# Performance work log

Hardware: AMD Instinct MI355X
Metric: run time of the kernel (lower is better)

## Reference

```python
import jax, jax.numpy as jnp
import numpy as np

N_NODES = 10000
N_EDGES = 320000
IN_DIM = 256
OUT_DIM = 256
N_REL = 16


def setup_inputs() -> dict:
    key = jax.random.key(0)
    k_x, k_src, k_dst, k_et, k_wr, k_w0 = jax.random.split(key, 6)
    x = jax.random.normal(k_x, (N_NODES, IN_DIM), dtype=jnp.float32)
    src = jax.random.randint(k_src, (N_EDGES,), 0, N_NODES)
    dst = jax.random.randint(k_dst, (N_EDGES,), 0, N_NODES)
    edge_index = jnp.stack([src, dst], axis=0)  # [2, E]
    edge_type = jax.random.randint(k_et, (N_EDGES,), 0, N_REL)
    # Xavier-uniform-ish init for weights
    lim_r = float(np.sqrt(6.0 / (IN_DIM + OUT_DIM)))
    W_r = jax.random.uniform(k_wr, (N_REL, IN_DIM, OUT_DIM), minval=-lim_r, maxval=lim_r, dtype=jnp.float32)
    W0_w = jax.random.uniform(k_w0, (OUT_DIM, IN_DIM), minval=-lim_r, maxval=lim_r, dtype=jnp.float32)
    W0_b = jnp.zeros((OUT_DIM,), dtype=jnp.float32)
    return {
        "x": x,
        "W_r": W_r,
        "W0_w": W0_w,
        "W0_b": W0_b,
        "edge_index": edge_index,
        "edge_type": edge_type,
        "num_nodes_local": N_NODES,
    }


def reference(x, W_r, W0_w, W0_b, edge_index, edge_type, num_nodes_local):
    N = num_nodes_local
    R = W_r.shape[0]
    src = edge_index[0]
    dst = edge_index[1]
    # Per-(relation, dst-node) in-degree, clamped at 1 (matches deg_r.clamp_min(1))
    deg = jnp.zeros((R, N), dtype=x.dtype).at[edge_type, dst].add(1.0)
    deg = jnp.maximum(deg, 1.0)  # [R, N]
    # Transform all nodes under every relation weight: grouped GEMM [R, N, out]
    h_all = jnp.einsum('nd,rdo->rno', x, W_r)
    # Gather per-edge message and normalize by relation-specific dst degree
    msg = h_all[edge_type, src] / deg[edge_type, dst][:, None]  # [E, out]
    # Scatter-add messages to destination nodes
    agg = jax.ops.segment_sum(msg, dst, num_segments=N)  # [N, out]
    # Self-loop transform W_0(x)
    return agg + x @ W0_w.T + W0_b
```

## Files before the change

kernel.cpp:

```cpp
#include <hip/hip_runtime.h>

typedef __bf16 bf16x8 __attribute__((ext_vector_type(8)));
typedef float f32x4 __attribute__((ext_vector_type(4)));

static __device__ __forceinline__ unsigned short f2bf(float f) {
    union { float f; unsigned int u; } v; v.f = f;
    unsigned int r = v.u + 0x7fffu + ((v.u >> 16) & 1u);
    return (unsigned short)(r >> 16);
}
static __device__ __forceinline__ float blo(unsigned int u) {
    union { unsigned int u; float f; } v; v.u = u << 16; return v.f;
}
static __device__ __forceinline__ float bhi(unsigned int u) {
    union { unsigned int u; float f; } v; v.u = u & 0xffff0000u; return v.f;
}
static __device__ __forceinline__ unsigned int pack2(float a, float b) {
    return (unsigned int)f2bf(a) | ((unsigned int)f2bf(b) << 16);
}

__global__ void zero_kernel(int* __restrict__ p, int n) {
    int i = blockIdx.x * blockDim.x + threadIdx.x;
    int n4 = n >> 2;
    if (i < n4) reinterpret_cast<int4*>(p)[i] = make_int4(0, 0, 0, 0);
    if (i < (n & 3)) p[(n4 << 2) + i] = 0;
}

__global__ void prep_kernel(const int* __restrict__ dst, const int* __restrict__ et,
                            int* __restrict__ deg,
                            const float* __restrict__ x, unsigned short* __restrict__ s,
                            int E, int N, int R, int nh) {
    const int bid = blockIdx.x, tid = threadIdx.x;
    const int K = (R + 1) * 256;
    if (bid < nh) {
        int i = bid * 256 + tid;
        if (i < E) atomicAdd(&deg[et[i] * N + dst[i]], 1);
    } else {
        int id = (bid - nh) * 256 + tid;
        int n = id >> 6, c4 = id & 63;
        if (n < N) {
            float4 v = *reinterpret_cast<const float4*>(&x[((size_t)n << 8) + (c4 << 2)]);
            ushort4 h;
            h.x = f2bf(v.x); h.y = f2bf(v.y); h.z = f2bf(v.z); h.w = f2bf(v.w);
            *reinterpret_cast<ushort4*>(&s[(size_t)n * K + (K - 256) + (c4 << 2)]) = h;
        }
    }
}

__global__ __launch_bounds__(256) void wtT_kernel(
    const float* __restrict__ Wr, const float* __restrict__ W0w,
    unsigned short* __restrict__ Wt2, int R, int K)
{
    __shared__ float t[64][65];
    const int sl = blockIdx.x, d0 = blockIdx.y * 64, o0 = blockIdx.z * 64;
    const int tid = threadIdx.x;
    if (sl < R) {
        #pragma unroll
        for (int j = 0; j < 16; ++j) {
            int idx = j * 256 + tid;
            int dr = idx >> 6, oc = idx & 63;
            t[dr][oc] = Wr[((size_t)sl * 256 + d0 + dr) * 256 + o0 + oc];
        }
        __syncthreads();
        #pragma unroll
        for (int j = 0; j < 4; ++j) {
            int idx = j * 256 + tid;
            int orow = idx >> 4, dc4 = (idx & 15) << 2;
            ushort4 h;
            h.x = f2bf(t[dc4 + 0][orow]); h.y = f2bf(t[dc4 + 1][orow]);
            h.z = f2bf(t[dc4 + 2][orow]); h.w = f2bf(t[dc4 + 3][orow]);
            *reinterpret_cast<ushort4*>(&Wt2[(size_t)(o0 + orow) * K + sl * 256 + d0 + dc4]) = h;
        }
    } else {
        #pragma unroll
        for (int j = 0; j < 4; ++j) {
            int idx = j * 256 + tid;
            int orow = idx >> 4, dc4 = (idx & 15) << 2;
            float4 v = *reinterpret_cast<const float4*>(&W0w[(size_t)(o0 + orow) * 256 + d0 + dc4]);
            ushort4 h;
            h.x = f2bf(v.x); h.y = f2bf(v.y); h.z = f2bf(v.z); h.w = f2bf(v.w);
            *reinterpret_cast<ushort4*>(&Wt2[(size_t)(o0 + orow) * K + sl * 256 + d0 + dc4]) = h;
        }
    }
}

__global__ void scan1_kernel(const int* __restrict__ deg, int* __restrict__ local,
                             int* __restrict__ bsum, int* __restrict__ ctr, int B) {
    __shared__ int tmp[256];
    int t = threadIdx.x, g = blockIdx.x * 256 + t;
    int v = (g < B) ? deg[g] : 0;
    tmp[t] = v; __syncthreads();
    for (int o = 1; o < 256; o <<= 1) {
        int u = (t >= o) ? tmp[t - o] : 0;
        __syncthreads();
        tmp[t] += u;
        __syncthreads();
    }
    if (g < B) { local[g] = tmp[t] - v; ctr[g] = 0; }
    if (t == 255) bsum[blockIdx.x] = tmp[t];
}

__global__ void scan2_kernel(const int* __restrict__ bsum, int* __restrict__ base, int nc) {
    __shared__ int tmp[1024];
    int t = threadIdx.x;
    int v = (t < nc) ? bsum[t] : 0;
    tmp[t] = v; __syncthreads();
    for (int o = 1; o < 1024; o <<= 1) {
        int u = (t >= o) ? tmp[t - o] : 0;
        __syncthreads();
        tmp[t] += u;
        __syncthreads();
    }
    if (t < nc) base[t] = tmp[t] - v;
}

__global__ void scatter_ids_kernel(const int* __restrict__ src, const int* __restrict__ dst,
                                   const int* __restrict__ et, const int* __restrict__ local,
                                   const int* __restrict__ base, int* __restrict__ ctr,
                                   int* __restrict__ srcs, int E, int N) {
    int i = blockIdx.x * blockDim.x + threadIdx.x;
    if (i < E) {
        int b = et[i] * N + dst[i];
        int p = local[b] + base[b >> 8] + atomicAdd(&ctr[b], 1);
        srcs[p] = src[i];
    }
}

__global__ __launch_bounds__(256) void reduce_kernel(
    const int* __restrict__ srcs, const int* __restrict__ deg,
    const int* __restrict__ local, const int* __restrict__ base,
    unsigned short* __restrict__ s, int N, int R)
{
    const int K = (R + 1) * 256;
    const int r = blockIdx.y;
    const int dn = blockIdx.x * 8 + (threadIdx.x >> 5);
    if (dn >= N) return;
    const int lane = threadIdx.x & 31;
    const int bin = r * N + dn;
    const int cnt = deg[bin];
    const int st  = local[bin] + base[bin >> 8];

    float a0 = 0.f, a1 = 0.f, a2 = 0.f, a3 = 0.f;
    float a4 = 0.f, a5 = 0.f, a6 = 0.f, a7 = 0.f;
    for (int c0 = 0; c0 < cnt; c0 += 32) {
        int sv = 0;
        if (c0 + lane < cnt) sv = srcs[st + c0 + lane];
        int m = cnt - c0; if (m > 32) m = 32;
        for (int i = 0; i < m; ++i) {
            int sn = __shfl(sv, i, 32);
            const uint4 v = *reinterpret_cast<const uint4*>(
                &s[(size_t)sn * K + (K - 256) + (lane << 3)]);
            a0 += blo(v.x); a1 += bhi(v.x);
            a2 += blo(v.y); a3 += bhi(v.y);
            a4 += blo(v.z); a5 += bhi(v.z);
            a6 += blo(v.w); a7 += bhi(v.w);
        }
    }
    if (cnt > 0) {
        float sc = 1.0f / (float)cnt;
        a0 *= sc; a1 *= sc; a2 *= sc; a3 *= sc;
        a4 *= sc; a5 *= sc; a6 *= sc; a7 *= sc;
    }
    uint4 o;
    o.x = pack2(a0, a1); o.y = pack2(a2, a3);
    o.z = pack2(a4, a5); o.w = pack2(a6, a7);
    *reinterpret_cast<uint4*>(&s[(size_t)dn * K + (r << 8) + (lane << 3)]) = o;
}

__global__ __launch_bounds__(256) void gemm_kernel(
    const unsigned short* __restrict__ S, const unsigned short* __restrict__ Wt2,
    const float* __restrict__ bias, float* __restrict__ dest,
    int M, int K, int ksteps, int addbias)
{
    __shared__ __align__(16) unsigned short ldsA[2][8192];
    __shared__ __align__(16) unsigned short ldsB[8192];
    const int tid = threadIdx.x;
    const int lane = tid & 63, w = tid >> 6;
    const int wm = w & 1, wn = w >> 1;
    const int m0 = blockIdx.x * 128, n0 = blockIdx.y * 128;
    const int kstart = blockIdx.z * ksteps * 64;
    const size_t rowb = (size_t)K * 2;

    f32x4 acc[4][4] = {};

    const int flat_base = w * 4 * 64 + lane;

#define STAGE_A(buf, kstep)                                                               \
    {                                                                                     \
        const int kb = (kstart + (kstep) * 64) * 2;                                       \
        _Pragma("unroll")                                                                 \
        for (int i = 0; i < 4; ++i) {                                                     \
            int flat = flat_base + i * 64;                                                \
            int row = flat >> 3, seg = flat & 7;                                          \
            int gr = m0 + row; gr = gr < M ? gr : M - 1;                                  \
            const char* gp = (const char*)S + (size_t)gr * rowb + kb                      \
                             + ((seg * 16) ^ ((row & 7) << 4));                           \
            unsigned short* lp = &ldsA[buf][(w * 4 + i) * 512];                           \
            __builtin_amdgcn_global_load_lds(                                             \
                (const __attribute__((address_space(1))) void*)gp,                        \
                (__attribute__((address_space(3))) void*)lp, 16, 0, 0);                   \
        }                                                                                 \
    }

#define STAGE_B(kstep)                                                                    \
    {                                                                                     \
        const int kb = (kstart + (kstep) * 64) * 2;                                       \
        _Pragma("unroll")                                                                 \
        for (int i = 0; i < 4; ++i) {                                                     \
            int flat = flat_base + i * 64;                                                \
            int row = flat >> 3, seg = flat & 7;                                          \
            const char* gp = (const char*)Wt2 + (size_t)(n0 + row) * rowb + kb            \
                             + ((seg * 16) ^ ((row & 7) << 4));                           \
            unsigned short* lp = &ldsB[(w * 4 + i) * 512];                                \
            __builtin_amdgcn_global_load_lds(                                             \
                (const __attribute__((address_space(1))) void*)gp,                        \
                (__attribute__((address_space(3))) void*)lp, 16, 0, 0);                   \
        }                                                                                 \
    }

#define COMPUTE(buf)                                                                      \
    {                                                                                     \
        _Pragma("unroll")                                                                 \
        for (int kk = 0; kk < 2; ++kk) {                                                  \
            bf16x8 af[4], bfr[4];                                                         \
            _Pragma("unroll")                                                             \
            for (int m = 0; m < 4; ++m) {                                                 \
                int row = wm * 64 + m * 16 + (lane & 15);                                 \
                int colb = (kk * 64 + ((lane >> 4) << 4)) ^ ((row & 7) << 4);             \
                af[m] = *reinterpret_cast<const bf16x8*>(                                 \
                    (const char*)&ldsA[buf][0] + row * 128 + colb);                       \
            }                                                                             \
            _Pragma("unroll")                                                             \
            for (int n = 0; n < 4; ++n) {                                                 \
                int row = wn * 64 + n * 16 + (lane & 15);                                 \
                int colb = (kk * 64 + ((lane >> 4) << 4)) ^ ((row & 7) << 4);             \
                bfr[n] = *reinterpret_cast<const bf16x8*>(                                \
                    (const char*)&ldsB[0] + row * 128 + colb);                            \
            }                                                                             \
            __builtin_amdgcn_s_setprio(1);                                                \
            _Pragma("unroll")                                                             \
            for (int m = 0; m < 4; ++m)                                                   \
                _Pragma("unroll")                                                         \
                for (int n = 0; n < 4; ++n)                                               \
                    acc[m][n] = __builtin_amdgcn_mfma_f32_16x16x32_bf16(                  \
                        af[m], bfr[n], acc[m][n], 0, 0, 0);                               \
            __builtin_amdgcn_s_setprio(0);                                                \
        }                                                                                 \
    }

    STAGE_A(0, 0)
    STAGE_B(0)
    STAGE_A(1, 1)
    asm volatile("s_waitcnt vmcnt(4)" ::: "memory");
    __builtin_amdgcn_s_barrier();

    for (int t = 0; t < ksteps; ++t) {
        COMPUTE(t & 1)
        asm volatile("s_waitcnt lgkmcnt(0)" ::: "memory");
        __builtin_amdgcn_sched_barrier(0);
        __builtin_amdgcn_s_barrier();
        if (t + 1 < ksteps) {
            STAGE_B(t + 1)
            if (t + 2 < ksteps) {
                STAGE_A(t & 1, t + 2)
                asm volatile("s_waitcnt vmcnt(4)" ::: "memory");
            } else {
                asm volatile("s_waitcnt vmcnt(0)" ::: "memory");
            }
            __builtin_amdgcn_s_barrier();
        }
    }
#undef STAGE_A
#undef STAGE_B
#undef COMPUTE

    float* dst = dest + (size_t)blockIdx.z * M * 256;
    const int rbase = m0 + wm * 64 + ((lane >> 4) << 2);
    const int cbase = n0 + wn * 64 + (lane & 15);
    #pragma unroll
    for (int n = 0; n < 4; ++n) {
        int c = cbase + n * 16;
        float bv = addbias ? bias[c] : 0.0f;
        #pragma unroll
        for (int m = 0; m < 4; ++m) {
            #pragma unroll
            for (int j = 0; j < 4; ++j) {
                int r = rbase + m * 16 + j;
                if (r < M) dst[(size_t)r * 256 + c] = acc[m][n][j] + bv;
            }
        }
    }
}

__global__ void combine_kernel(const float* __restrict__ pbuf, const float* __restrict__ bias,
                               float* __restrict__ out, int M, int KZ) {
    int id = blockIdx.x * blockDim.x + threadIdx.x;
    if (id >= M * 64) return;
    int n = id >> 6, c4 = id & 63;
    float4 a = *reinterpret_cast<const float4*>(&pbuf[((size_t)n << 8) + (c4 << 2)]);
    for (int kz = 1; kz < KZ; ++kz) {
        float4 b = *reinterpret_cast<const float4*>(&pbuf[(size_t)kz * M * 256 + ((size_t)n << 8) + (c4 << 2)]);
        a.x += b.x; a.y += b.y; a.z += b.z; a.w += b.w;
    }
    const float4 bv = *reinterpret_cast<const float4*>(&bias[c4 << 2]);
    a.x += bv.x; a.y += bv.y; a.z += bv.z; a.w += bv.w;
    *reinterpret_cast<float4*>(&out[((size_t)n << 8) + (c4 << 2)]) = a;
}

extern "C" void kernel_launch(void* const* d_in, const int* in_sizes, int n_in,
                              void* d_out, int out_size, void* d_ws, size_t ws_size,
                              hipStream_t stream) {
    const float* x   = (const float*)d_in[0];
    const float* Wr  = (const float*)d_in[1];
    const float* W0w = (const float*)d_in[2];
    const float* W0b = (const float*)d_in[3];
    const int*   eidx= (const int*)d_in[4];
    const int*   et  = (const int*)d_in[5];
    const int N = in_sizes[0] / 256;
    const int R = in_sizes[1] / 65536;
    const int E = in_sizes[5];
    const int* src = eidx;
    const int* dst = eidx + E;
    float* out = (float*)d_out;

    const int B = R * N;
    const int NC = (B + 255) / 256;
    const int K = (R + 1) * 256;

    const size_t sz_pslice = (size_t)N * 256 * 4;
    const size_t sz_sort = (((size_t)B * 4 + 255) & ~255UL) * 3
                         + (((size_t)E * 4 + 255) & ~255UL)
                         + 2 * 4096;
    const size_t sz_wt2 = (size_t)256 * K * 2;
    const size_t sz_s   = (size_t)N * K * 2;
    int KZ = 1;
    for (int kz = 4; kz >= 1; kz >>= 1) {
        size_t r0 = (kz > 1) ? (size_t)kz * sz_pslice : 0;
        if (sz_sort > r0) r0 = sz_sort;
        size_t need = ((r0 + 255) & ~255UL) + ((sz_wt2 + 255) & ~255UL) + sz_s + 1024;
        if (need <= ws_size || kz == 1) { KZ = kz; break; }
    }

    char* ws = (char*)d_ws;
    size_t off = 0;
    auto alloc = [&](size_t bytes) { void* p = ws + off; off = (off + bytes + 255) & ~(size_t)255; return p; };
    float* pbuf = (float*)ws;
    int* deg    = (int*)alloc((size_t)B * 4);
    int* local  = (int*)alloc((size_t)B * 4);
    int* bsum   = (int*)alloc(4096);
    int* base   = (int*)alloc(4096);
    int* ctr    = (int*)alloc((size_t)B * 4);
    int* srcs   = (int*)alloc((size_t)E * 4);
    size_t region0 = (KZ > 1) ? (size_t)KZ * sz_pslice : 0;
    if (off > region0) region0 = off;
    off = (region0 + 255) & ~(size_t)255;
    unsigned short* Wt2 = (unsigned short*)alloc(sz_wt2);
    unsigned short* s   = (unsigned short*)alloc(sz_s);

    zero_kernel<<<(B / 4 + 255) / 256, 256, 0, stream>>>(deg, B);
    {
        const int nh = (E + 255) / 256;
        const int nx = (N * 64 + 255) / 256;
        prep_kernel<<<nh + nx, 256, 0, stream>>>(dst, et, deg, x, s, E, N, R, nh);
    }
    {
        dim3 gw(R + 1, 4, 4);
        wtT_kernel<<<gw, 256, 0, stream>>>(Wr, W0w, Wt2, R, K);
    }
    scan1_kernel<<<NC, 256, 0, stream>>>(deg, local, bsum, ctr, B);
    scan2_kernel<<<1, 1024, 0, stream>>>(bsum, base, NC);
    scatter_ids_kernel<<<(E + 255) / 256, 256, 0, stream>>>(src, dst, et, local, base, ctr, srcs, E, N);
    {
        dim3 g((N + 7) / 8, R);
        reduce_kernel<<<g, 256, 0, stream>>>(srcs, deg, local, base, s, N, R);
    }
    {
        const int ktot = K / 64;
        const int ksteps = ktot / KZ;
        dim3 grid((N + 127) / 128, 2, KZ);
        if (KZ == 1) {
            gemm_kernel<<<grid, 256, 0, stream>>>(s, Wt2, W0b, out, N, K, ksteps, 1);
        } else {
            gemm_kernel<<<grid, 256, 0, stream>>>(s, Wt2, W0b, pbuf, N, K, ksteps, 0);
            combine_kernel<<<(N * 64 + 255) / 256, 256, 0, stream>>>(pbuf, W0b, out, N, KZ);
        }
    }
}
```

Baseline: 134.1 us.

## Merge weight transpose into prep, fuse scans, store split-K partials in bf16

Folds the weight transpose into the prep kernel and records each edge's slot offset from the degree atomic. That removes the separate counter array and the second atomic pass in scatter. The two scan kernels become one, where the last block to finish (found via an atomic ticket) scans the block sums. Split-K partial outputs are stored as bf16 instead of fp32 to halve combine traffic, at some cost in accuracy.

Result: slower. 174.1 us (+29.8%).

```diff
diff --git a/kernel.cpp b/kernel.cpp
--- a/kernel.cpp
+++ b/kernel.cpp
@@ -25,16 +25,24 @@
     if (i < (n & 3)) p[(n4 << 2) + i] = 0;
 }
 
-__global__ void prep_kernel(const int* __restrict__ dst, const int* __restrict__ et,
-                            int* __restrict__ deg,
-                            const float* __restrict__ x, unsigned short* __restrict__ s,
-                            int E, int N, int R, int nh) {
+__global__ __launch_bounds__(256) void prep_kernel(
+    const int* __restrict__ dst, const int* __restrict__ et,
+    int* __restrict__ deg, int* __restrict__ eoff,
+    const float* __restrict__ x, unsigned short* __restrict__ s,
+    const float* __restrict__ Wr, const float* __restrict__ W0w,
+    unsigned short* __restrict__ Wt2,
+    int E, int N, int R, int nh, int nx)
+{
+    __shared__ float t[64][65];
     const int bid = blockIdx.x, tid = threadIdx.x;
     const int K = (R + 1) * 256;
     if (bid < nh) {
         int i = bid * 256 + tid;
-        if (i < E) atomicAdd(&deg[et[i] * N + dst[i]], 1);
-    } else {
+        if (i < E) {
+            int b = et[i] * N + dst[i];
+            eoff[i] = atomicAdd(&deg[b], 1);
+        }
+    } else if (bid < nh + nx) {
         int id = (bid - nh) * 256 + tid;
         int n = id >> 6, c4 = id & 63;
         if (n < N) {
@@ -43,49 +51,45 @@
             h.x = f2bf(v.x); h.y = f2bf(v.y); h.z = f2bf(v.z); h.w = f2bf(v.w);
             *reinterpret_cast<ushort4*>(&s[(size_t)n * K + (K - 256) + (c4 << 2)]) = h;
         }
-    }
-}
-
-__global__ __launch_bounds__(256) void wtT_kernel(
-    const float* __restrict__ Wr, const float* __restrict__ W0w,
-    unsigned short* __restrict__ Wt2, int R, int K)
-{
-    __shared__ float t[64][65];
-    const int sl = blockIdx.x, d0 = blockIdx.y * 64, o0 = blockIdx.z * 64;
-    const int tid = threadIdx.x;
-    if (sl < R) {
-        #pragma unroll
-        for (int j = 0; j < 16; ++j) {
-            int idx = j * 256 + tid;
-            int dr = idx >> 6, oc = idx & 63;
-            t[dr][oc] = Wr[((size_t)sl * 256 + d0 + dr) * 256 + o0 + oc];
-        }
-        __syncthreads();
-        #pragma unroll
-        for (int j = 0; j < 4; ++j) {
-            int idx = j * 256 + tid;
-            int orow = idx >> 4, dc4 = (idx & 15) << 2;
-            ushort4 h;
-            h.x = f2bf(t[dc4 + 0][orow]); h.y = f2bf(t[dc4 + 1][orow]);
-            h.z = f2bf(t[dc4 + 2][orow]); h.w = f2bf(t[dc4 + 3][orow]);
-            *reinterpret_cast<ushort4*>(&Wt2[(size_t)(o0 + orow) * K + sl * 256 + d0 + dc4]) = h;
-        }
     } else {
-        #pragma unroll
-        for (int j = 0; j < 4; ++j) {
-            int idx = j * 256 + tid;
-            int orow = idx >> 4, dc4 = (idx & 15) << 2;
-            float4 v = *reinterpret_cast<const float4*>(&W0w[(size_t)(o0 + orow) * 256 + d0 + dc4]);
-            ushort4 h;
-            h.x = f2bf(v.x); h.y = f2bf(v.y); h.z = f2bf(v.z); h.w = f2bf(v.w);
-            *reinterpret_cast<ushort4*>(&Wt2[(size_t)(o0 + orow) * K + sl * 256 + d0 + dc4]) = h;
-        }
-    }
-}
-
-__global__ void scan1_kernel(const int* __restrict__ deg, int* __restrict__ local,
-                             int* __restrict__ bsum, int* __restrict__ ctr, int B) {
+        int tb = bid - nh - nx;
+        int sl = tb >> 4, d0 = ((tb >> 2) & 3) * 64, o0 = (tb & 3) * 64;
+        if (sl < R) {
+            #pragma unroll
+            for (int j = 0; j < 16; ++j) {
+                int idx = j * 256 + tid;
+                int dr = idx >> 6, oc = idx & 63;
+                t[dr][oc] = Wr[((size_t)sl * 256 + d0 + dr) * 256 + o0 + oc];
+            }
+            __syncthreads();
+            #pragma unroll
+            for (int j = 0; j < 4; ++j) {
+                int idx = j * 256 + tid;
+                int orow = idx >> 4, dc4 = (idx & 15) << 2;
+                ushort4 h;
+                h.x = f2bf(t[dc4 + 0][orow]); h.y = f2bf(t[dc4 + 1][orow]);
+                h.z = f2bf(t[dc4 + 2][orow]); h.w = f2bf(t[dc4 + 3][orow]);
+                *reinterpret_cast<ushort4*>(&Wt2[(size_t)(o0 + orow) * K + sl * 256 + d0 + dc4]) = h;
+            }
+        } else {
+            #pragma unroll
+            for (int j = 0; j < 4; ++j) {
+                int idx = j * 256 + tid;
+                int orow = idx >> 4, dc4 = (idx & 15) << 2;
+                float4 v = *reinterpret_cast<const float4*>(&W0w[(size_t)(o0 + orow) * 256 + d0 + dc4]);
+                ushort4 h;
+                h.x = f2bf(v.x); h.y = f2bf(v.y); h.z = f2bf(v.z); h.w = f2bf(v.w);
+                *reinterpret_cast<ushort4*>(&Wt2[(size_t)(o0 + orow) * K + sl * 256 + d0 + dc4]) = h;
+            }
+        }
+    }
+}
+
+__global__ void scan_kernel(const int* __restrict__ deg, int* __restrict__ local,
+                            int* __restrict__ bsum, int* __restrict__ base,
+                            int* __restrict__ tick, int B, int NC) {
     __shared__ int tmp[256];
+    __shared__ int sflag, carry;
     int t = threadIdx.x, g = blockIdx.x * 256 + t;
     int v = (g < B) ? deg[g] : 0;
     tmp[t] = v; __syncthreads();
@@ -95,33 +99,40 @@
         tmp[t] += u;
         __syncthreads();
     }
-    if (g < B) { local[g] = tmp[t] - v; ctr[g] = 0; }
+    if (g < B) local[g] = tmp[t] - v;
     if (t == 255) bsum[blockIdx.x] = tmp[t];
-}
-
-__global__ void scan2_kernel(const int* __restrict__ bsum, int* __restrict__ base, int nc) {
-    __shared__ int tmp[1024];
-    int t = threadIdx.x;
-    int v = (t < nc) ? bsum[t] : 0;
-    tmp[t] = v; __syncthreads();
-    for (int o = 1; o < 1024; o <<= 1) {
-        int u = (t >= o) ? tmp[t - o] : 0;
+    __threadfence();
+    if (t == 0) sflag = (atomicAdd(tick, 1) == (int)gridDim.x - 1) ? 1 : 0;
+    __syncthreads();
+    if (sflag) {
+        __threadfence();
+        if (t == 0) carry = 0;
         __syncthreads();
-        tmp[t] += u;
-        __syncthreads();
-    }
-    if (t < nc) base[t] = tmp[t] - v;
+        for (int c0 = 0; c0 < NC; c0 += 256) {
+            int w = (c0 + t < NC) ? bsum[c0 + t] : 0;
+            tmp[t] = w; __syncthreads();
+            for (int o = 1; o < 256; o <<= 1) {
+                int u = (t >= o) ? tmp[t - o] : 0;
+                __syncthreads();
+                tmp[t] += u;
+                __syncthreads();
+            }
+            if (c0 + t < NC) base[c0 + t] = tmp[t] - w + carry;
+            __syncthreads();
+            if (t == 0) carry += tmp[255];
+            __syncthreads();
+        }
+    }
 }
 
 __global__ void scatter_ids_kernel(const int* __restrict__ src, const int* __restrict__ dst,
                                    const int* __restrict__ et, const int* __restrict__ local,
-                                   const int* __restrict__ base, int* __restrict__ ctr,
+                                   const int* __restrict__ base, const int* __restrict__ eoff,
                                    int* __restrict__ srcs, int E, int N) {
     int i = blockIdx.x * blockDim.x + threadIdx.x;
     if (i < E) {
         int b = et[i] * N + dst[i];
-        int p = local[b] + base[b >> 8] + atomicAdd(&ctr[b], 1);
-        srcs[p] = src[i];
+        srcs[local[b] + base[b >> 8] + eoff[i]] = src[i];
     }
 }
 
@@ -168,7 +179,7 @@
 
 __global__ __launch_bounds__(256) void gemm_kernel(
     const unsigned short* __restrict__ S, const unsigned short* __restrict__ Wt2,
-    const float* __restrict__ bias, float* __restrict__ dest,
+    const float* __restrict__ bias, void* __restrict__ dest,
     int M, int K, int ksteps, int addbias)
 {
     __shared__ __align__(16) unsigned short ldsA[2][8192];
@@ -273,36 +284,52 @@
 #undef STAGE_B
 #undef COMPUTE
 
-    float* dst = dest + (size_t)blockIdx.z * M * 256;
     const int rbase = m0 + wm * 64 + ((lane >> 4) << 2);
     const int cbase = n0 + wn * 64 + (lane & 15);
-    #pragma unroll
-    for (int n = 0; n < 4; ++n) {
-        int c = cbase + n * 16;
-        float bv = addbias ? bias[c] : 0.0f;
+    if (addbias) {
+        float* dst = (float*)dest;
         #pragma unroll
-        for (int m = 0; m < 4; ++m) {
+        for (int n = 0; n < 4; ++n) {
+            int c = cbase + n * 16;
+            float bv = bias[c];
             #pragma unroll
-            for (int j = 0; j < 4; ++j) {
-                int r = rbase + m * 16 + j;
-                if (r < M) dst[(size_t)r * 256 + c] = acc[m][n][j] + bv;
-            }
-        }
-    }
-}
-
-__global__ void combine_kernel(const float* __restrict__ pbuf, const float* __restrict__ bias,
+            for (int m = 0; m < 4; ++m)
+                #pragma unroll
+                for (int j = 0; j < 4; ++j) {
+                    int r = rbase + m * 16 + j;
+                    if (r < M) dst[(size_t)r * 256 + c] = acc[m][n][j] + bv;
+                }
+        }
+    } else {
+        unsigned short* dst = (unsigned short*)dest + (size_t)blockIdx.z * M * 256;
+        #pragma unroll
+        for (int n = 0; n < 4; ++n) {
+            int c = cbase + n * 16;
+            #pragma unroll
+            for (int m = 0; m < 4; ++m)
+                #pragma unroll
+                for (int j = 0; j < 4; ++j) {
+                    int r = rbase + m * 16 + j;
+                    if (r < M) dst[(size_t)r * 256 + c] = f2bf(acc[m][n][j]);
+                }
+        }
+    }
+}
+
+__global__ void combine_kernel(const unsigned short* __restrict__ pbuf,
+                               const float* __restrict__ bias,
                                float* __restrict__ out, int M, int KZ) {
     int id = blockIdx.x * blockDim.x + threadIdx.x;
     if (id >= M * 64) return;
     int n = id >> 6, c4 = id & 63;
-    float4 a = *reinterpret_cast<const float4*>(&pbuf[((size_t)n << 8) + (c4 << 2)]);
-    for (int kz = 1; kz < KZ; ++kz) {
-        float4 b = *reinterpret_cast<const float4*>(&pbuf[(size_t)kz * M * 256 + ((size_t)n << 8) + (c4 << 2)]);
-        a.x += b.x; a.y += b.y; a.z += b.z; a.w += b.w;
-    }
     const float4 bv = *reinterpret_cast<const float4*>(&bias[c4 << 2]);
-    a.x += bv.x; a.y += bv.y; a.z += bv.z; a.w += bv.w;
+    float4 a = bv;
+    for (int kz = 0; kz < KZ; ++kz) {
+        uint2 v = *reinterpret_cast<const uint2*>(
+            &pbuf[(size_t)kz * M * 256 + ((size_t)n << 8) + (c4 << 2)]);
+        a.x += blo(v.x); a.y += bhi(v.x);
+        a.z += blo(v.y); a.w += bhi(v.y);
+    }
     *reinterpret_cast<float4*>(&out[((size_t)n << 8) + (c4 << 2)]) = a;
 }
 
@@ -326,9 +353,10 @@
     const int NC = (B + 255) / 256;
     const int K = (R + 1) * 256;
 
-    const size_t sz_pslice = (size_t)N * 256 * 4;
-    const size_t sz_sort = (((size_t)B * 4 + 255) & ~255UL) * 3
-                         + (((size_t)E * 4 + 255) & ~255UL)
+    const size_t sz_pslice = (size_t)N * 256 * 2;
+    const size_t sz_sort = (((size_t)(B + 8) * 4 + 255) & ~255UL)
+                         + (((size_t)B * 4 + 255) & ~255UL)
+                         + (((size_t)E * 4 + 255) & ~255UL) * 2
                          + 2 * 4096;
     const size_t sz_wt2 = (size_t)256 * K * 2;
     const size_t sz_s   = (size_t)N * K * 2;
@@ -343,12 +371,13 @@
     char* ws = (char*)d_ws;
     size_t off = 0;
     auto alloc = [&](size_t bytes) { void* p = ws + off; off = (off + bytes + 255) & ~(size_t)255; return p; };
-    float* pbuf = (float*)ws;
-    int* deg    = (int*)alloc((size_t)B * 4);
+    unsigned short* pbuf = (unsigned short*)ws;
+    int* deg    = (int*)alloc((size_t)(B + 8) * 4);
+    int* tick   = deg + B;
     int* local  = (int*)alloc((size_t)B * 4);
     int* bsum   = (int*)alloc(4096);
     int* base   = (int*)alloc(4096);
-    int* ctr    = (int*)alloc((size_t)B * 4);
+    int* eoff   = (int*)alloc((size_t)E * 4);
     int* srcs   = (int*)alloc((size_t)E * 4);
     size_t region0 = (KZ > 1) ? (size_t)KZ * sz_pslice : 0;
     if (off > region0) region0 = off;
@@ -356,19 +385,16 @@
     unsigned short* Wt2 = (unsigned short*)alloc(sz_wt2);
     unsigned short* s   = (unsigned short*)alloc(sz_s);
 
-    zero_kernel<<<(B / 4 + 255) / 256, 256, 0, stream>>>(deg, B);
+    zero_kernel<<<((B + 8) / 4 + 255) / 256, 256, 0, stream>>>(deg, B + 8);
     {
         const int nh = (E + 255) / 256;
         const int nx = (N * 64 + 255) / 256;
-        prep_kernel<<<nh + nx, 256, 0, stream>>>(dst, et, deg, x, s, E, N, R, nh);
-    }
-    {
-        dim3 gw(R + 1, 4, 4);
-        wtT_kernel<<<gw, 256, 0, stream>>>(Wr, W0w, Wt2, R, K);
-    }
-    scan1_kernel<<<NC, 256, 0, stream>>>(deg, local, bsum, ctr, B);
-    scan2_kernel<<<1, 1024, 0, stream>>>(bsum, base, NC);
-    scatter_ids_kernel<<<(E + 255) / 256, 256, 0, stream>>>(src, dst, et, local, base, ctr, srcs, E, N);
+        const int nwT = (R + 1) * 16;
+        prep_kernel<<<nh + nx + nwT, 256, 0, stream>>>(dst, et, deg, eoff, x, s,
+                                                       Wr, W0w, Wt2, E, N, R, nh, nx);
+    }
+    scan_kernel<<<NC, 256, 0, stream>>>(deg, local, bsum, base, tick, B, NC);
+    scatter_ids_kernel<<<(E + 255) / 256, 256, 0, stream>>>(src, dst, et, local, base, eoff, srcs, E, N);
     {
         dim3 g((N + 7) / 8, R);
         reduce_kernel<<<g, 256, 0, stream>>>(srcs, deg, local, base, s, N, R);
@@ -378,9 +404,9 @@
         const int ksteps = ktot / KZ;
         dim3 grid((N + 127) / 128, 2, KZ);
         if (KZ == 1) {
-            gemm_kernel<<<grid, 256, 0, stream>>>(s, Wt2, W0b, out, N, K, ksteps, 1);
+            gemm_kernel<<<grid, 256, 0, stream>>>(s, Wt2, W0b, (void*)out, N, K, ksteps, 1);
         } else {
-            gemm_kernel<<<grid, 256, 0, stream>>>(s, Wt2, W0b, pbuf, N, K, ksteps, 0);
+            gemm_kernel<<<grid, 256, 0, stream>>>(s, Wt2, W0b, (void*)pbuf, N, K, ksteps, 0);
             combine_kernel<<<(N * 64 + 255) / 256, 256, 0, stream>>>(pbuf, W0b, out, N, KZ);
         }
     }
```

## Load GEMM operands directly from global memory instead of LDS staging

Applied to the files above, without the earlier changes.

Removes the double-buffered LDS staging (global_load_lds plus barriers) in the bf16 GEMM kernel, so each wave reads its MFMA fragments straight from global memory through per-row pointers. This drops LDS traffic and block-wide synchronisation, relying on the caches to serve the reuse across waves. The cost is redundant global/L2 reads, since every wave refetches its A and B rows, and no explicit prefetch overlap. It also redirects output to the base buffer when addbias is set.

After: 195.0 us. +45.4%, slower.

```diff
diff --git a/kernel.cpp b/kernel.cpp
--- a/kernel.cpp
+++ b/kernel.cpp
@@ -171,109 +171,53 @@
     const float* __restrict__ bias, float* __restrict__ dest,
     int M, int K, int ksteps, int addbias)
 {
-    __shared__ __align__(16) unsigned short ldsA[2][8192];
-    __shared__ __align__(16) unsigned short ldsB[8192];
     const int tid = threadIdx.x;
     const int lane = tid & 63, w = tid >> 6;
     const int wm = w & 1, wn = w >> 1;
     const int m0 = blockIdx.x * 128, n0 = blockIdx.y * 128;
     const int kstart = blockIdx.z * ksteps * 64;
-    const size_t rowb = (size_t)K * 2;
+    const int l15 = lane & 15, lq = lane >> 4;
 
     f32x4 acc[4][4] = {};
 
-    const int flat_base = w * 4 * 64 + lane;
-
-#define STAGE_A(buf, kstep)                                                               \
-    {                                                                                     \
-        const int kb = (kstart + (kstep) * 64) * 2;                                       \
-        _Pragma("unroll")                                                                 \
-        for (int i = 0; i < 4; ++i) {                                                     \
-            int flat = flat_base + i * 64;                                                \
-            int row = flat >> 3, seg = flat & 7;                                          \
-            int gr = m0 + row; gr = gr < M ? gr : M - 1;                                  \
-            const char* gp = (const char*)S + (size_t)gr * rowb + kb                      \
-                             + ((seg * 16) ^ ((row & 7) << 4));                           \
-            unsigned short* lp = &ldsA[buf][(w * 4 + i) * 512];                           \
-            __builtin_amdgcn_global_load_lds(                                             \
-                (const __attribute__((address_space(1))) void*)gp,                        \
-                (__attribute__((address_space(3))) void*)lp, 16, 0, 0);                   \
-        }                                                                                 \
-    }
-
-#define STAGE_B(kstep)                                                                    \
-    {                                                                                     \
-        const int kb = (kstart + (kstep) * 64) * 2;                                       \
-        _Pragma("unroll")                                                                 \
-        for (int i = 0; i < 4; ++i) {                                                     \
-            int flat = flat_base + i * 64;                                                \
-            int row = flat >> 3, seg = flat & 7;                                          \
-            const char* gp = (const char*)Wt2 + (size_t)(n0 + row) * rowb + kb            \
-                             + ((seg * 16) ^ ((row & 7) << 4));                           \
-            unsigned short* lp = &ldsB[(w * 4 + i) * 512];                                \
-            __builtin_amdgcn_global_load_lds(                                             \
-                (const __attribute__((address_space(1))) void*)gp,                        \
-                (__attribute__((address_space(3))) void*)lp, 16, 0, 0);                   \
-        }                                                                                 \
-    }
-
-#define COMPUTE(buf)                                                                      \
-    {                                                                                     \
-        _Pragma("unroll")                                                                 \
-        for (int kk = 0; kk < 2; ++kk) {                                                  \
-            bf16x8 af[4], bfr[4];                                                         \
-            _Pragma("unroll")                                                             \
-            for (int m = 0; m < 4; ++m) {                                                 \
-                int row = wm * 64 + m * 16 + (lane & 15);                                 \
-                int colb = (kk * 64 + ((lane >> 4) << 4)) ^ ((row & 7) << 4);             \
-                af[m] = *reinterpret_cast<const bf16x8*>(                                 \
-                    (const char*)&ldsA[buf][0] + row * 128 + colb);                       \
-            }                                                                             \
-            _Pragma("unroll")                                                             \
-            for (int n = 0; n < 4; ++n) {                                                 \
-                int row = wn * 64 + n * 16 + (lane & 15);                                 \
-                int colb = (kk * 64 + ((lane >> 4) << 4)) ^ ((row & 7) << 4);             \
-                bfr[n] = *reinterpret_cast<const bf16x8*>(                                \
-                    (const char*)&ldsB[0] + row * 128 + colb);                            \
-            }                                                                             \
-            __builtin_amdgcn_s_setprio(1);                                                \
-            _Pragma("unroll")                                                             \
-            for (int m = 0; m < 4; ++m)                                                   \
-                _Pragma("unroll")                                                         \
-                for (int n = 0; n < 4; ++n)                                               \
-                    acc[m][n] = __builtin_amdgcn_mfma_f32_16x16x32_bf16(                  \
-                        af[m], bfr[n], acc[m][n], 0, 0, 0);                               \
-            __builtin_amdgcn_s_setprio(0);                                                \
-        }                                                                                 \
-    }
-
-    STAGE_A(0, 0)
-    STAGE_B(0)
-    STAGE_A(1, 1)
-    asm volatile("s_waitcnt vmcnt(4)" ::: "memory");
-    __builtin_amdgcn_s_barrier();
+    const unsigned short* aptr[4];
+    const unsigned short* bptr[4];
+    #pragma unroll
+    for (int m = 0; m < 4; ++m) {
+        int gr = m0 + wm * 64 + m * 16 + l15;
+        gr = gr < M ? gr : M - 1;
+        aptr[m] = S + (size_t)gr * K + kstart + lq * 8;
+    }
+    #pragma unroll
+    for (int n = 0; n < 4; ++n) {
+        int r = n0 + wn * 64 + n * 16 + l15;
+        bptr[n] = Wt2 + (size_t)r * K + kstart + lq * 8;
+    }
 
     for (int t = 0; t < ksteps; ++t) {
-        COMPUTE(t & 1)
-        asm volatile("s_waitcnt lgkmcnt(0)" ::: "memory");
-        __builtin_amdgcn_sched_barrier(0);
-        __builtin_amdgcn_s_barrier();
-        if (t + 1 < ksteps) {
-            STAGE_B(t + 1)
-            if (t + 2 < ksteps) {
-                STAGE_A(t & 1, t + 2)
-                asm volatile("s_waitcnt vmcnt(4)" ::: "memory");
-            } else {
-                asm volatile("s_waitcnt vmcnt(0)" ::: "memory");
-            }
-            __builtin_amdgcn_s_barrier();
-        }
-    }
-#undef STAGE_A
-#undef STAGE_B
-#undef COMPUTE
+        const int k0 = t * 64;
+        #pragma unroll
+        for (int kk = 0; kk < 2; ++kk) {
+            bf16x8 af[4], bfr[4];
+            #pragma unroll
+            for (int m = 0; m < 4; ++m)
+                af[m] = *reinterpret_cast<const bf16x8*>(aptr[m] + k0 + kk * 32);
+            #pragma unroll
+            for (int n = 0; n < 4; ++n)
+                bfr[n] = *reinterpret_cast<const bf16x8*>(bptr[n] + k0 + kk * 32);
+            __builtin_amdgcn_s_setprio(1);
+            #pragma unroll
+            for (int m = 0; m < 4; ++m)
+                #pragma unroll
+                for (int n = 0; n < 4; ++n)
+                    acc[m][n] = __builtin_amdgcn_mfma_f32_16x16x32_bf16(
+                        af[m], bfr[n], acc[m][n], 0, 0, 0);
+            __builtin_amdgcn_s_setprio(0);
+        }
+    }
 
     float* dst = dest + (size_t)blockIdx.z * M * 256;
+    if (addbias) dst = dest;
     const int rbase = m0 + wm * 64 + ((lane >> 4) << 2);
     const int cbase = n0 + wn * 64 + (lane & 15);
     #pragma unroll
```
